# Kernel tuning notes

Measured on AMD Instinct MI355X. Metric: run time of the kernel, lower is better.

Reference implementation:

```python
import jax, jax.numpy as jnp
import numpy as np

N = 500000   # num_nodes
K = 32       # ring buffer slots (max_neighbors)
B = 8192     # event batch size
D = 128      # memory_dim == embedding_dim == attention input_dim
T = 64       # time_dim
H = 2        # num_heads
KS = 16      # top-k sampled neighbors per query


def time_encode(dt, w, b):
    # Time2Vec: sin on even channels, cos on odd channels. dt [...], w/b [T]
    f = dt[..., None] * w + b
    even = (jnp.arange(w.shape[0]) % 2) == 0
    return jnp.where(even, jnp.sin(f), jnp.cos(f))


def setup_inputs() -> dict:
    key = jax.random.key(0)
    ks = jax.random.split(key, 40)
    def rn(i, shape, s=0.05):
        return jax.random.normal(ks[i], shape, dtype=jnp.float32) * s
    inp = {}
    inp["src"] = jax.random.randint(ks[0], (B,), 0, N)
    inp["dst"] = jax.random.randint(ks[1], (B,), 0, N)
    # shift query timestamps so every row has valid (earlier) neighbors w.h.p.
    inp["ts"] = 0.5 + 0.5 * jax.random.uniform(ks[2], (B,), dtype=jnp.float32)
    inp["nbr_ids"] = jax.random.randint(ks[3], (N, K), 0, N, dtype=jnp.int32)
    inp["nbr_ts"] = jax.random.uniform(ks[4], (N, K), dtype=jnp.float32)
    inp["memory"] = rn(5, (N, D), 0.1)
    inp["last_update"] = jnp.zeros((N,), jnp.float32)
    # message function: TimeEncoding + MLP(2*D + T -> D -> D)
    inp["w_t_msg"] = rn(6, (T,), 0.1); inp["b_t_msg"] = jnp.zeros((T,), jnp.float32)
    inp["W_msg1"] = rn(7, (D, 2 * D + T)); inp["b_msg1"] = jnp.zeros((D,), jnp.float32)
    inp["W_msg2"] = rn(8, (D, D)); inp["b_msg2"] = jnp.zeros((D,), jnp.float32)
    # GRUCell(message_dim=D, memory_dim=D)
    inp["W_ih"] = rn(9, (3 * D, D)); inp["b_ih"] = jnp.zeros((3 * D,), jnp.float32)
    inp["W_hh"] = rn(10, (3 * D, D)); inp["b_hh"] = jnp.zeros((3 * D,), jnp.float32)
    # temporal attention
    inp["w_t_att"] = rn(11, (T,), 0.1); inp["b_t_att"] = jnp.zeros((T,), jnp.float32)
    inp["Wq"] = rn(12, (D, D)); inp["bq"] = jnp.zeros((D,), jnp.float32)
    inp["Wk"] = rn(13, (D, D + T)); inp["bk"] = jnp.zeros((D,), jnp.float32)
    inp["Wv"] = rn(14, (D, D + T)); inp["bv"] = jnp.zeros((D,), jnp.float32)
    inp["Wo"] = rn(15, (D, D)); inp["bo"] = jnp.zeros((D,), jnp.float32)
    # merge MLP(D + D -> D -> D) + layernorm
    inp["Wm1"] = rn(16, (D, 2 * D)); inp["bm1"] = jnp.zeros((D,), jnp.float32)
    inp["Wm2"] = rn(17, (D, D)); inp["bm2"] = jnp.zeros((D,), jnp.float32)
    inp["ln_g"] = jnp.ones((D,), jnp.float32); inp["ln_b"] = jnp.zeros((D,), jnp.float32)
    return inp


def reference(src, dst, ts, nbr_ids, nbr_ts, memory, last_update,
              w_t_msg, b_t_msg, W_msg1, b_msg1, W_msg2, b_msg2,
              W_ih, b_ih, W_hh, b_hh,
              w_t_att, b_t_att, Wq, bq, Wk, bk, Wv, bv, Wo, bo,
              Wm1, bm1, Wm2, bm2, ln_g, ln_b):
    # ---- C1: message computation + GRU memory scatter-update (both endpoints) ----
    nodes = jnp.concatenate([src, dst])        # [2B]
    others = jnp.concatenate([dst, src])
    tb = jnp.concatenate([ts, ts])
    self_mem = memory[nodes]                   # [2B, D] gather
    oth_mem = memory[others]
    dt = tb - last_update[nodes]
    te = time_encode(dt, w_t_msg, b_t_msg)     # [2B, T]
    x = jnp.concatenate([self_mem, oth_mem, te], axis=-1)
    msg = jax.nn.relu(x @ W_msg1.T + b_msg1) @ W_msg2.T + b_msg2   # [2B, D]
    # GRUCell
    gi = msg @ W_ih.T + b_ih
    gh = self_mem @ W_hh.T + b_hh
    ir, iz, ig = jnp.split(gi, 3, axis=-1)
    hr, hz, hg = jnp.split(gh, 3, axis=-1)
    r = jax.nn.sigmoid(ir + hr)
    z = jax.nn.sigmoid(iz + hz)
    g = jnp.tanh(ig + r * hg)
    new_mem = (1.0 - z) * g + z * self_mem
    mem2 = memory.at[nodes].set(new_mem)       # scatter-update

    # ---- temporal top-k neighbor sampling for src queries ----
    ids = nbr_ids[src]                         # [B, K]
    nts = nbr_ts[src]                          # [B, K]
    valid = (ids >= 0) & (nts < ts[:, None] + 1e-6)
    sort_ts = jnp.where(valid, nts, -1e30)
    _, idx = jax.lax.top_k(sort_ts, KS)        # most recent first
    sel_ids = jnp.take_along_axis(ids, idx, axis=1)
    sel_ts = jnp.take_along_axis(nts, idx, axis=1)
    mk = jnp.take_along_axis(valid, idx, axis=1)
    tdelta = jnp.where(mk, ts[:, None] - sel_ts, 0.0)
    sel_ids = jnp.clip(jnp.where(mk, sel_ids, 0), 0, N - 1)

    # ---- temporal attention embedding layer ----
    nbr_feat = mem2[sel_ids]                   # [B, KS, D] gather
    node_feat = mem2[src]                      # [B, D]
    te_a = time_encode(tdelta, w_t_att, b_t_att)        # [B, KS, T]
    kv = jnp.concatenate([nbr_feat, te_a], axis=-1)     # [B, KS, D+T]
    hd = D // H
    Q = (node_feat @ Wq.T + bq).reshape(B, H, hd)
    Kp = (kv @ Wk.T + bk).reshape(B, KS, H, hd).transpose(0, 2, 1, 3)
    Vp = (kv @ Wv.T + bv).reshape(B, KS, H, hd).transpose(0, 2, 1, 3)
    scores = jnp.einsum('bhd,bhnd->bhn', Q, Kp) / jnp.sqrt(jnp.float32(hd))
    scores = jnp.where(mk[:, None, :], scores, -jnp.inf)
    attn = jnp.nan_to_num(jax.nn.softmax(scores, axis=-1), nan=0.0)
    out = jnp.einsum('bhn,bhnd->bhd', attn, Vp).reshape(B, D)
    attn_out = out @ Wo.T + bo
    # merge with memory + layernorm
    comb = jnp.concatenate([attn_out, node_feat], axis=-1)
    h = jax.nn.relu(comb @ Wm1.T + bm1) @ Wm2.T + bm2
    mu = h.mean(axis=-1, keepdims=True)
    var = ((h - mu) ** 2).mean(axis=-1, keepdims=True)
    emb = (h - mu) / jnp.sqrt(var + 1e-5) * ln_g + ln_b   # [B, D]
    return emb
```

## Files before the change

### kernel.cpp

```cpp
#include <hip/hip_runtime.h>
#include <math.h>

#define BATCH  8192
#define NNODES 500000
#define DIM    128
#define TDIM   64
#define KNB    32
#define KSEL   16

#define OFF_W1   0
#define OFF_W2   40960
#define OFF_WIH  57344
#define OFF_WHH  106496
#define OFF_WQ   155648
#define OFF_WV   172032
#define OFF_WO   196608
#define OFF_WM1  212992
#define OFF_WM2  245760
#define OFF_WKT  262144
#define CVT_TOT  286720

#define NB_CVT  1120
#define NB_WIN  (NB_CVT + 64)
#define NB_TOPK (NB_WIN + 32)

typedef float  f32x4  __attribute__((ext_vector_type(4)));
typedef __bf16 bf16x8 __attribute__((ext_vector_type(8)));
typedef short  s16x8  __attribute__((ext_vector_type(8)));

#define MFMA(a,b,c) __builtin_amdgcn_mfma_f32_16x16x32_bf16(a,b,c,0,0,0)

__device__ __forceinline__ float rcpf_(float x) { return __builtin_amdgcn_rcpf(x); }
__device__ __forceinline__ float fsigmoid(float x) { return rcpf_(1.f + __expf(-x)); }
__device__ __forceinline__ float ftanh(float x) {
    float e = __expf(2.f * x);
    return 1.f - 2.f * rcpf_(e + 1.f);
}
__device__ __forceinline__ unsigned short f2bf(float x) {
    unsigned u = __builtin_bit_cast(unsigned, x);
    unsigned r = (u + 0x7FFFu + ((u >> 16) & 1u)) >> 16;
    return (unsigned short)r;
}
__device__ __forceinline__ float bf2f(unsigned short u) {
    unsigned v = ((unsigned)u) << 16;
    return __builtin_bit_cast(float, v);
}
__device__ __forceinline__ bf16x8 ldfrag(const unsigned short* p) {
    s16x8 v = *(const s16x8*)p;
    return __builtin_bit_cast(bf16x8, v);
}
__device__ __forceinline__ uint2 pack4bf(float4 v) {
    uint2 pk;
    pk.x = (unsigned)f2bf(v.x) | ((unsigned)f2bf(v.y) << 16);
    pk.y = (unsigned)f2bf(v.z) | ((unsigned)f2bf(v.w) << 16);
    return pk;
}

__global__ __launch_bounds__(256) void k_prep(
    const float* __restrict__ sW1, const float* __restrict__ sW2,
    const float* __restrict__ sWih, const float* __restrict__ sWhh,
    const float* __restrict__ sWq, const float* __restrict__ sWv,
    const float* __restrict__ sWo, const float* __restrict__ sWm1,
    const float* __restrict__ sWm2, const float* __restrict__ sWk,
    unsigned short* __restrict__ pool,
    const int* __restrict__ src, const int* __restrict__ dst,
    int* __restrict__ winner,
    const float* __restrict__ ts,
    const int* __restrict__ nbr_ids, const float* __restrict__ nbr_ts,
    int* __restrict__ sel_id, float* __restrict__ sel_td, int* __restrict__ sel_mk)
{
    const int bid = blockIdx.x;
    const int tid = threadIdx.x;

    if (bid < NB_CVT) {
        int i = bid * 256 + tid;
        float v;
        if      (i < OFF_W2)  { v = sW1 [i - OFF_W1 ]; }
        else if (i < OFF_WIH) { v = sW2 [i - OFF_W2 ]; }
        else if (i < OFF_WHH) { v = sWih[i - OFF_WIH]; }
        else if (i < OFF_WQ)  { v = sWhh[i - OFF_WHH]; }
        else if (i < OFF_WV)  { v = sWq [i - OFF_WQ ]; }
        else if (i < OFF_WO)  { v = sWv [i - OFF_WV ]; }
        else if (i < OFF_WM1) { v = sWo [i - OFF_WO ]; }
        else if (i < OFF_WM2) { v = sWm1[i - OFF_WM1]; }
        else if (i < OFF_WKT) { v = sWm2[i - OFF_WM2]; }
        else {
            int j = i - OFF_WKT;
            int h = j / 12288, rem = j % 12288;
            int c = rem >> 6, dh = rem & 63;
            v = sWk[(size_t)(h * 64 + dh) * 192 + c];
        }
        pool[i] = f2bf(v);
        return;
    }
    if (bid < NB_WIN) {
        int i = (bid - NB_CVT) * 256 + tid;
        if (i < 2 * BATCH) {
            int v = (i < BATCH) ? src[i] : dst[i - BATCH];
            atomicMax(&winner[v], i);
        }
        return;
    }
    {
        int b = (bid - NB_WIN) * 256 + tid;
        if (b >= BATCH) return;
        int   s = src[b];
        float t = ts[b];
        const int4*   ip4 = (const int4*)  (nbr_ids + (size_t)s * KNB);
        const float4* tp4 = (const float4*)(nbr_ts  + (size_t)s * KNB);
        float kt[KNB]; int kid[KNB];
        #pragma unroll
        for (int j4 = 0; j4 < 8; ++j4) {
            int4   id4 = ip4[j4];
            float4 nt4 = tp4[j4];
            int   ids[4] = { id4.x, id4.y, id4.z, id4.w };
            float nts[4] = { nt4.x, nt4.y, nt4.z, nt4.w };
            #pragma unroll
            for (int q = 0; q < 4; ++q) {
                int j = j4 * 4 + q;
                bool valid = (ids[q] >= 0) && (nts[q] < t + 1e-6f);
                kt[j]  = valid ? nts[q] : -1e30f;
                kid[j] = ids[q];
            }
        }
        unsigned picked = 0u;
        for (int sI = 0; sI < KSEL; ++sI) {
            float bv = -3.4e38f; int bj = 0; int bid2 = 0;
            #pragma unroll
            for (int j = 0; j < KNB; ++j) {
                bool avail = !((picked >> j) & 1u);
                if (avail && kt[j] > bv) { bv = kt[j]; bj = j; bid2 = kid[j]; }
            }
            picked |= (1u << bj);
            bool mk = bv > -1e29f;
            int id = mk ? (bid2 < 0 ? 0 : (bid2 > NNODES - 1 ? NNODES - 1 : bid2)) : 0;
            sel_id[b * KSEL + sI] = id;
            sel_td[b * KSEL + sI] = mk ? (t - bv) : 0.f;
            sel_mk[b * KSEL + sI] = mk ? 1 : 0;
        }
    }
}

__global__ __launch_bounds__(512) void k1_mfma(
    const int* __restrict__ src, const int* __restrict__ dst, const float* __restrict__ ts,
    const float* __restrict__ memory, const float* __restrict__ last_update,
    const float* __restrict__ w_t, const float* __restrict__ b_t,
    const unsigned short* __restrict__ Wp,
    const float* __restrict__ b1, const float* __restrict__ b2,
    const float* __restrict__ bih, const float* __restrict__ bhh,
    float* __restrict__ new_mem)
{
    __shared__ unsigned short sxb[64][328];
    __shared__ unsigned short hb [64][136];
    __shared__ int   s_node[64];
    __shared__ int   s_oth [64];
    __shared__ float s_dt  [64];

    const unsigned short* W1b  = Wp + OFF_W1;
    const unsigned short* W2b  = Wp + OFF_W2;
    const unsigned short* Wihb = Wp + OFF_WIH;
    const unsigned short* Whhb = Wp + OFF_WHH;

    const int tid  = threadIdx.x;
    const int base = blockIdx.x * 64;

    if (tid < 64) {
        int gi = base + tid;
        int node, oth; float t;
        if (gi < BATCH) { node = src[gi];         oth = dst[gi];         t = ts[gi]; }
        else            { node = dst[gi - BATCH]; oth = src[gi - BATCH]; t = ts[gi - BATCH]; }
        s_node[tid] = node;
        s_oth[tid]  = oth;
        s_dt[tid]   = t - last_update[node];
    }
    __syncthreads();

    for (int idx = tid; idx < 64 * 32; idx += 512) {
        int r = idx >> 5, c4 = (idx & 31) << 2;
        float4 vs = *(const float4*)&memory[(size_t)s_node[r] * DIM + c4];
        float4 vo = *(const float4*)&memory[(size_t)s_oth[r]  * DIM + c4];
        *(uint2*)&sxb[r][c4]       = pack4bf(vs);
        *(uint2*)&sxb[r][128 + c4] = pack4bf(vo);
    }
    for (int idx = tid; idx < 64 * TDIM; idx += 512) {
        int r = idx >> 6, c = idx & 63;
        float f = s_dt[r] * w_t[c] + b_t[c];
        sxb[r][256 + c] = f2bf((c & 1) ? __cosf(f) : __sinf(f));
    }
    __syncthreads();

    const int w    = tid >> 6;
    const int l    = tid & 63;
    const int rowA = l & 15;
    const int kg   = l >> 4;
    const int n0   = w * 16;
    const int col  = l & 15;
    const int rgrp = l >> 4;

    {
        f32x4 a0 = {0.f,0.f,0.f,0.f}, a1 = {0.f,0.f,0.f,0.f};
        f32x4 a2 = {0.f,0.f,0.f,0.f}, a3 = {0.f,0.f,0.f,0.f};
        #pragma unroll
        for (int kt = 0; kt < 10; ++kt) {
            int ko = kt * 32 + kg * 8;
            bf16x8 bfr = ldfrag(&W1b[(size_t)(n0 + rowA) * 320 + ko]);
            a0 = MFMA(ldfrag(&sxb[     rowA][ko]), bfr, a0);
            a1 = MFMA(ldfrag(&sxb[16 + rowA][ko]), bfr, a1);
            a2 = MFMA(ldfrag(&sxb[32 + rowA][ko]), bfr, a2);
            a3 = MFMA(ldfrag(&sxb[48 + rowA][ko]), bfr, a3);
        }
        float bb = b1[n0 + col];
        #pragma unroll
        for (int rgi = 0; rgi < 4; ++rgi) {
            int rb = rgrp * 4 + rgi;
            hb[rb     ][n0 + col] = f2bf(fmaxf(a0[rgi] + bb, 0.f));
            hb[rb + 16][n0 + col] = f2bf(fmaxf(a1[rgi] + bb, 0.f));
            hb[rb + 32][n0 + col] = f2bf(fmaxf(a2[rgi] + bb, 0.f));
            hb[rb + 48][n0 + col] = f2bf(fmaxf(a3[rgi] + bb, 0.f));
        }
    }
    __syncthreads();

    {
        f32x4 m0 = {0.f,0.f,0.f,0.f}, m1 = {0.f,0.f,0.f,0.f};
        f32x4 m2 = {0.f,0.f,0.f,0.f}, m3 = {0.f,0.f,0.f,0.f};
        #pragma unroll
        for (int kt = 0; kt < 4; ++kt) {
            int ko = kt * 32 + kg * 8;
            bf16x8 bfr = ldfrag(&W2b[(size_t)(n0 + rowA) * 128 + ko]);
            m0 = MFMA(ldfrag(&hb[     rowA][ko]), bfr, m0);
            m1 = MFMA(ldfrag(&hb[16 + rowA][ko]), bfr, m1);
            m2 = MFMA(ldfrag(&hb[32 + rowA][ko]), bfr, m2);
            m3 = MFMA(ldfrag(&hb[48 + rowA][ko]), bfr, m3);
        }
        __syncthreads();
        float bb = b2[n0 + col];
        #pragma unroll
        for (int rgi = 0; rgi < 4; ++rgi) {
            int rb = rgrp * 4 + rgi;
            hb[rb     ][n0 + col] = f2bf(m0[rgi] + bb);
            hb[rb + 16][n0 + col] = f2bf(m1[rgi] + bb);
            hb[rb + 32][n0 + col] = f2bf(m2[rgi] + bb);
            hb[rb + 48][n0 + col] = f2bf(m3[rgi] + bb);
        }
    }
    __syncthreads();

    {
        f32x4 g[6][4];
        #pragma unroll
        for (int gi_ = 0; gi_ < 6; ++gi_)
            #pragma unroll
            for (int ta = 0; ta < 4; ++ta) g[gi_][ta] = (f32x4){0.f,0.f,0.f,0.f};
        #pragma unroll
        for (int kt = 0; kt < 4; ++kt) {
            int ko = kt * 32 + kg * 8;
            int br = n0 + rowA;
            bf16x8 bir = ldfrag(&Wihb[(size_t)(      br) * 128 + ko]);
            bf16x8 biz = ldfrag(&Wihb[(size_t)(128 + br) * 128 + ko]);
            bf16x8 big = ldfrag(&Wihb[(size_t)(256 + br) * 128 + ko]);
            bf16x8 bhr = ldfrag(&Whhb[(size_t)(      br) * 128 + ko]);
            bf16x8 bhz = ldfrag(&Whhb[(size_t)(128 + br) * 128 + ko]);
            bf16x8 bhg = ldfrag(&Whhb[(size_t)(256 + br) * 128 + ko]);
            #pragma unroll
            for (int ta = 0; ta < 4; ++ta) {
                bf16x8 am = ldfrag(&hb [ta * 16 + rowA][ko]);
                bf16x8 ah = ldfrag(&sxb[ta * 16 + rowA][ko]);
                g[0][ta] = MFMA(am, bir, g[0][ta]);
                g[1][ta] = MFMA(am, biz, g[1][ta]);
                g[2][ta] = MFMA(am, big, g[2][ta]);
                g[3][ta] = MFMA(ah, bhr, g[3][ta]);
                g[4][ta] = MFMA(ah, bhz, g[4][ta]);
                g[5][ta] = MFMA(ah, bhg, g[5][ta]);
            }
        }
        const int d = n0 + col;
        float bir = bih[d], biz = bih[128 + d], big = bih[256 + d];
        float bhr = bhh[d], bhz = bhh[128 + d], bhg = bhh[256 + d];
        #pragma unroll
        for (int ta = 0; ta < 4; ++ta)
            #pragma unroll
            for (int rgi = 0; rgi < 4; ++rgi) {
                int rr = ta * 16 + rgrp * 4 + rgi;
                float rv = fsigmoid((g[0][ta][rgi] + bir) + (g[3][ta][rgi] + bhr));
                float zv = fsigmoid((g[1][ta][rgi] + biz) + (g[4][ta][rgi] + bhz));
                float gv = ftanh((g[2][ta][rgi] + big) + rv * (g[5][ta][rgi] + bhg));
                float selfv = bf2f(sxb[rr][d]);
                new_mem[(size_t)(base + rr) * DIM + d] = (1.f - zv) * gv + zv * selfv;
            }
    }
}

__global__ __launch_bounds__(512) void k3_fused(
    const int* __restrict__ src,
    const float* __restrict__ memory, const float* __restrict__ new_mem,
    const int* __restrict__ winner,
    const int* __restrict__ sel_id, const float* __restrict__ sel_td,
    const int* __restrict__ sel_mk,
    const float* __restrict__ w_ta, const float* __restrict__ b_ta,
    const unsigned short* __restrict__ Wp,
    const float* __restrict__ bq, const float* __restrict__ bk,
    const float* __restrict__ bv, const float* __restrict__ bo,
    const float* __restrict__ bm1, const float* __restrict__ bm2,
    const float* __restrict__ ln_g, const float* __restrict__ ln_b,
    float* __restrict__ out)
{
    __shared__ unsigned short s_nfB[32][136];
    __shared__ unsigned short s_qB [32][136];
    __shared__ unsigned short s_u  [32][2][200];
    __shared__ unsigned short s_kvb[32][2][200];
    __shared__ unsigned long long s_pool64[6400];
    __shared__ const float* s_nptr[32][16];
    __shared__ float s_td [32][16];
    __shared__ int   s_mk [32][16];
    __shared__ float s_qb [32][2];
    __shared__ float s_satt[32][2];
    __shared__ float s_at [8][2][16];
    __shared__ const float* s_ptr[32];

    const unsigned short* Wqb  = Wp + OFF_WQ;
    const unsigned short* WkTb = Wp + OFF_WKT;
    const unsigned short* Wvb  = Wp + OFF_WV;
    const unsigned short* Wob  = Wp + OFF_WO;
    const unsigned short* Wm1b = Wp + OFF_WM1;
    const unsigned short* Wm2b = Wp + OFF_WM2;

    const int tid  = threadIdx.x;
    const int base = blockIdx.x * 32;

    if (tid < 32) {
        int v = src[base + tid];
        int wv = winner[v];
        s_ptr[tid] = (wv >= 0) ? (new_mem + (size_t)wv * DIM)
                               : (memory  + (size_t)v  * DIM);
    }
    {
        int r = tid >> 4, n = tid & 15;
        int id = sel_id[(base + r) * KSEL + n];
        int wi = winner[id];
        s_nptr[r][n] = (wi >= 0) ? (new_mem + (size_t)wi * DIM)
                                 : (memory  + (size_t)id * DIM);
        s_td[r][n] = sel_td[(base + r) * KSEL + n];
        s_mk[r][n] = sel_mk[(base + r) * KSEL + n];
    }
    __syncthreads();

    for (int idx = tid; idx < 32 * 32; idx += 512) {
        int r = idx >> 5, c4 = (idx & 31) << 2;
        float4 v = *(const float4*)&s_ptr[r][c4];
        *(uint2*)&s_nfB[r][c4] = pack4bf(v);
    }
    __syncthreads();

    const int w    = tid >> 6;
    const int l    = tid & 63;
    const int rowA = l & 15;
    const int kg   = l >> 4;
    const int col  = l & 15;
    const int rgrp = l >> 4;

    {
        const int n0 = w * 16;
        f32x4 q0 = {0.f,0.f,0.f,0.f}, q1 = {0.f,0.f,0.f,0.f};
        #pragma unroll
        for (int kt = 0; kt < 4; ++kt) {
            int ko = kt * 32 + kg * 8;
            bf16x8 bfr = ldfrag(&Wqb[(size_t)(n0 + rowA) * 128 + ko]);
            q0 = MFMA(ldfrag(&s_nfB[     rowA][ko]), bfr, q0);
            q1 = MFMA(ldfrag(&s_nfB[16 + rowA][ko]), bfr, q1);
        }
        float bb = bq[n0 + col];
        #pragma unroll
        for (int rgi = 0; rgi < 4; ++rgi) {
            int rb = rgrp * 4 + rgi;
            s_qB[rb     ][n0 + col] = f2bf(q0[rgi] + bb);
            s_qB[rb + 16][n0 + col] = f2bf(q1[rgi] + bb);
        }
    }
    __syncthreads();

    if (tid < 256) {
        int r = tid >> 3, rem = tid & 7, h = rem >> 2, p = rem & 3;
        float part = 0.f;
        #pragma unroll
        for (int j = 0; j < 16; ++j) {
            int dd = h * 64 + p * 16 + j;
            part += bf2f(s_qB[r][dd]) * bk[dd];
        }
        part += __shfl_xor(part, 1);
        part += __shfl_xor(part, 2);
        if (p == 0) s_qb[r][h] = part;
    }

    {
        const int h  = w >> 2;
        const int cb = (w & 3) * 48;
        f32x4 u[3][2];
        #pragma unroll
        for (int ct = 0; ct < 3; ++ct)
            #pragma unroll
            for (int ta = 0; ta < 2; ++ta) u[ct][ta] = (f32x4){0.f,0.f,0.f,0.f};
        #pragma unroll
        for (int kt = 0; kt < 2; ++kt) {
            int ko = kt * 32 + kg * 8;
            bf16x8 bfr[3];
            #pragma unroll
            for (int ct = 0; ct < 3; ++ct)
                bfr[ct] = ldfrag(&WkTb[(size_t)h * 12288 + (size_t)(cb + ct * 16 + rowA) * 64 + ko]);
            #pragma unroll
            for (int ta = 0; ta < 2; ++ta) {
                bf16x8 av = ldfrag(&s_qB[ta * 16 + rowA][h * 64 + ko]);
                #pragma unroll
                for (int ct = 0; ct < 3; ++ct)
                    u[ct][ta] = MFMA(av, bfr[ct], u[ct][ta]);
            }
        }
        #pragma unroll
        for (int ct = 0; ct < 3; ++ct)
            #pragma unroll
            for (int ta = 0; ta < 2; ++ta)
                #pragma unroll
                for (int rgi = 0; rgi < 4; ++rgi) {
                    int rr = ta * 16 + rgrp * 4 + rgi;
                    s_u[rr][h][cb + ct * 16 + col] = f2bf(u[ct][ta][rgi]);
                }
    }
    __syncthreads();

    {
        unsigned short (*kvbuf)[16][200] = (unsigned short (*)[16][200])s_pool64;
        float wt = w_ta[l], bt = b_ta[l];
        const int pfn = l >> 5;
        const int pfc = (l & 31) << 2;

        float4 pf[8];
        {
            const int r = w * 4;
            #pragma unroll
            for (int it = 0; it < 8; ++it)
                pf[it] = *(const float4*)&s_nptr[r][it * 2 + pfn][pfc];
        }

        for (int rr = 0; rr < 4; ++rr) {
            const int r = w * 4 + rr;
            #pragma unroll
            for (int it = 0; it < 8; ++it)
                *(uint2*)&kvbuf[w][it * 2 + pfn][pfc] = pack4bf(pf[it]);
            #pragma unroll
            for (int n = 0; n < 16; ++n) {
                float f = s_td[r][n] * wt + bt;
                kvbuf[w][n][128 + l] = f2bf((l & 1) ? __cosf(f) : __sinf(f));
            }
            if (rr < 3) {
                const int rn = r + 1;
                #pragma unroll
                for (int it = 0; it < 8; ++it)
                    pf[it] = *(const float4*)&s_nptr[rn][it * 2 + pfn][pfc];
            }
            __builtin_amdgcn_wave_barrier();

            {
                int h = (l >> 4) & 1, n = l & 15, half = l >> 5;
                float acc = (half == 0) ? s_qb[r][h] : 0.f;
                const unsigned short* kvrow = &kvbuf[w][n][half * 96];
                const unsigned short* urow  = &s_u[r][h][half * 96];
                #pragma unroll
                for (int k = 0; k < 96; k += 8) {
                    s16x8 kv8 = *(const s16x8*)&kvrow[k];
                    s16x8 u8  = *(const s16x8*)&urow[k];
                    #pragma unroll
                    for (int j = 0; j < 8; ++j)
                        acc += bf2f((unsigned short)kv8[j]) * bf2f((unsigned short)u8[j]);
                }
                acc += __shfl_xor(acc, 32);
                int mk = s_mk[r][n];
                float s = mk ? acc * 0.125f : -INFINITY;
                float mx = s;
                #pragma unroll
                for (int m = 1; m < 16; m <<= 1) mx = fmaxf(mx, __shfl_xor(mx, m));
                float p = (mk && mx > -1e37f) ? __expf(s - mx) : 0.f;
                float den = p;
                #pragma unroll
                for (int m = 1; m < 16; m <<= 1) den += __shfl_xor(den, m);
                float a = (den > 0.f) ? (p * rcpf_(den)) : 0.f;
                if (l < 32) s_at[w][h][n] = a;
                if (l == 0 || l == 16) s_satt[r][h] = (den > 0.f) ? 1.f : 0.f;
            }
            __builtin_amdgcn_wave_barrier();

            #pragma unroll
            for (int i = 0; i < 3; ++i) {
                int c = i * 64 + l;
                float k0 = 0.f, k1 = 0.f;
                #pragma unroll
                for (int n = 0; n < 16; ++n) {
                    float v = bf2f(kvbuf[w][n][c]);
                    k0 += s_at[w][0][n] * v;
                    k1 += s_at[w][1][n] * v;
                }
                s_kvb[r][0][c] = f2bf(k0);
                s_kvb[r][1][c] = f2bf(k1);
            }
            __builtin_amdgcn_wave_barrier();
        }
    }
    __syncthreads();

    unsigned short (*s_aoB)[136] = (unsigned short (*)[136])s_pool64;
    unsigned short (*s_oB )[136] = (unsigned short (*)[136])((char*)s_pool64 + 8704);
    unsigned short (*s_h1B)[136] = (unsigned short (*)[136])((char*)s_pool64 + 17408);
    float          (*s_h2 )[128] = (float          (*)[128])((char*)s_pool64 + 26112);

    {
        const int h  = w >> 2;
        const int c0 = (w & 3) * 16;
        f32x4 o0 = {0.f,0.f,0.f,0.f}, o1 = {0.f,0.f,0.f,0.f};
        #pragma unroll
        for (int kt = 0; kt < 6; ++kt) {
            int ko = kt * 32 + kg * 8;
            bf16x8 bfr = ldfrag(&Wvb[(size_t)(h * 64 + c0 + rowA) * 192 + ko]);
            o0 = MFMA(ldfrag(&s_kvb[     rowA][h][ko]), bfr, o0);
            o1 = MFMA(ldfrag(&s_kvb[16 + rowA][h][ko]), bfr, o1);
        }
        int d0 = h * 64 + c0 + col;
        float bv0 = bv[d0];
        #pragma unroll
        for (int rgi = 0; rgi < 4; ++rgi) {
            int rb = rgrp * 4 + rgi;
            s_oB[rb     ][d0] = f2bf(o0[rgi] + s_satt[rb     ][h] * bv0);
            s_oB[rb + 16][d0] = f2bf(o1[rgi] + s_satt[rb + 16][h] * bv0);
        }
    }
    __syncthreads();

    {
        const int n0 = w * 16;
        f32x4 a0 = {0.f,0.f,0.f,0.f}, a1 = {0.f,0.f,0.f,0.f};
        #pragma unroll
        for (int kt = 0; kt < 4; ++kt) {
            int ko = kt * 32 + kg * 8;
            bf16x8 bfr = ldfrag(&Wob[(size_t)(n0 + rowA) * 128 + ko]);
            a0 = MFMA(ldfrag(&s_oB[     rowA][ko]), bfr, a0);
            a1 = MFMA(ldfrag(&s_oB[16 + rowA][ko]), bfr, a1);
        }
        float bb = bo[n0 + col];
        #pragma unroll
        for (int rgi = 0; rgi < 4; ++rgi) {
            int rb = rgrp * 4 + rgi;
            s_aoB[rb     ][n0 + col] = f2bf(a0[rgi] + bb);
            s_aoB[rb + 16][n0 + col] = f2bf(a1[rgi] + bb);
        }
    }
    __syncthreads();

    {
        const int n0 = w * 16;
        f32x4 a0 = {0.f,0.f,0.f,0.f}, a1 = {0.f,0.f,0.f,0.f};
        #pragma unroll
        for (int kt = 0; kt < 8; ++kt) {
            int ko = kt * 32 + kg * 8;
            bf16x8 av0 = (kt < 4) ? ldfrag(&s_aoB[     rowA][ko])
                                  : ldfrag(&s_nfB[     rowA][ko - 128]);
            bf16x8 av1 = (kt < 4) ? ldfrag(&s_aoB[16 + rowA][ko])
                                  : ldfrag(&s_nfB[16 + rowA][ko - 128]);
            bf16x8 bfr = ldfrag(&Wm1b[(size_t)(n0 + rowA) * 256 + ko]);
            a0 = MFMA(av0, bfr, a0);
            a1 = MFMA(av1, bfr, a1);
        }
        float bb = bm1[n0 + col];
        #pragma unroll
        for (int rgi = 0; rgi < 4; ++rgi) {
            int rb = rgrp * 4 + rgi;
            s_h1B[rb     ][n0 + col] = f2bf(fmaxf(a0[rgi] + bb, 0.f));
            s_h1B[rb + 16][n0 + col] = f2bf(fmaxf(a1[rgi] + bb, 0.f));
        }
    }
    __syncthreads();

    {
        const int n0 = w * 16;
        f32x4 a0 = {0.f,0.f,0.f,0.f}, a1 = {0.f,0.f,0.f,0.f};
        #pragma unroll
        for (int kt = 0; kt < 4; ++kt) {
            int ko = kt * 32 + kg * 8;
            bf16x8 bfr = ldfrag(&Wm2b[(size_t)(n0 + rowA) * 128 + ko]);
            a0 = MFMA(ldfrag(&s_h1B[     rowA][ko]), bfr, a0);
            a1 = MFMA(ldfrag(&s_h1B[16 + rowA][ko]), bfr, a1);
        }
        float bb = bm2[n0 + col];
        #pragma unroll
        for (int rgi = 0; rgi < 4; ++rgi) {
            int rb = rgrp * 4 + rgi;
            s_h2[rb     ][n0 + col] = a0[rgi] + bb;
            s_h2[rb + 16][n0 + col] = a1[rgi] + bb;
        }
    }
    __syncthreads();

    {
        float lg0 = ln_g[l], lg1 = ln_g[64 + l];
        float lb0 = ln_b[l], lb1 = ln_b[64 + l];
        #pragma unroll
        for (int i = 0; i < 4; ++i) {
            int r = w * 4 + i;
            float v0 = s_h2[r][l], v1 = s_h2[r][64 + l];
            float sum = v0 + v1;
            #pragma unroll
            for (int m = 1; m < 64; m <<= 1) sum += __shfl_xor(sum, m);
            float mean = sum * (1.f / 128.f);
            float e0 = v0 - mean, e1 = v1 - mean;
            float sq = e0 * e0 + e1 * e1;
            #pragma unroll
            for (int m = 1; m < 64; m <<= 1) sq += __shfl_xor(sq, m);
            float inv = rsqrtf(sq * (1.f / 128.f) + 1e-5f);
            out[(size_t)(base + r) * DIM + l]      = e0 * inv * lg0 + lb0;
            out[(size_t)(base + r) * DIM + 64 + l] = e1 * inv * lg1 + lb1;
        }
    }
}

extern "C" void kernel_launch(void* const* d_in, const int* in_sizes, int n_in,
                              void* d_out, int out_size, void* d_ws, size_t ws_size,
                              hipStream_t stream) {
    const int*   src         = (const int*)  d_in[0];
    const int*   dst         = (const int*)  d_in[1];
    const float* ts          = (const float*)d_in[2];
    const int*   nbr_ids     = (const int*)  d_in[3];
    const float* nbr_ts      = (const float*)d_in[4];
    const float* memory      = (const float*)d_in[5];
    const float* last_update = (const float*)d_in[6];
    const float* w_t_msg     = (const float*)d_in[7];
    const float* b_t_msg     = (const float*)d_in[8];
    const float* W_msg1      = (const float*)d_in[9];
    const float* b_msg1      = (const float*)d_in[10];
    const float* W_msg2      = (const float*)d_in[11];
    const float* b_msg2      = (const float*)d_in[12];
    const float* W_ih        = (const float*)d_in[13];
    const float* b_ih        = (const float*)d_in[14];
    const float* W_hh        = (const float*)d_in[15];
    const float* b_hh        = (const float*)d_in[16];
    const float* w_t_att     = (const float*)d_in[17];
    const float* b_t_att     = (const float*)d_in[18];
    const float* Wq          = (const float*)d_in[19];
    const float* bq          = (const float*)d_in[20];
    const float* Wk          = (const float*)d_in[21];
    const float* bk          = (const float*)d_in[22];
    const float* Wv          = (const float*)d_in[23];
    const float* bv          = (const float*)d_in[24];
    const float* Wo          = (const float*)d_in[25];
    const float* bo          = (const float*)d_in[26];
    const float* Wm1         = (const float*)d_in[27];
    const float* bm1         = (const float*)d_in[28];
    const float* Wm2         = (const float*)d_in[29];
    const float* bm2         = (const float*)d_in[30];
    const float* ln_g        = (const float*)d_in[31];
    const float* ln_b        = (const float*)d_in[32];
    float* out = (float*)d_out;

    char* ws = (char*)d_ws;
    size_t off = 0;
    float* new_mem = (float*)(ws + off); off += (size_t)2 * BATCH * DIM * 4;
    int*   winner  = (int*)  (ws + off); off += 2097152;
    int*   sel_id  = (int*)  (ws + off); off += (size_t)BATCH * KSEL * 4;
    float* sel_td  = (float*)(ws + off); off += (size_t)BATCH * KSEL * 4;
    int*   sel_mk  = (int*)  (ws + off); off += (size_t)BATCH * KSEL * 4;
    unsigned short* Wpool = (unsigned short*)(ws + off); off += (size_t)CVT_TOT * 2;

    hipMemsetAsync(winner, 0xFF, NNODES * sizeof(int), stream);
    k_prep<<<NB_TOPK, 256, 0, stream>>>(
        W_msg1, W_msg2, W_ih, W_hh, Wq, Wv, Wo, Wm1, Wm2, Wk, Wpool,
        src, dst, winner, ts, nbr_ids, nbr_ts, sel_id, sel_td, sel_mk);
    k1_mfma<<<(2 * BATCH) / 64, 512, 0, stream>>>(
        src, dst, ts, memory, last_update,
        w_t_msg, b_t_msg, Wpool, b_msg1, b_msg2, b_ih, b_hh, new_mem);
    k3_fused<<<BATCH / 32, 512, 0, stream>>>(
        src, memory, new_mem, winner, sel_id, sel_td, sel_mk,
        w_t_att, b_t_att, Wpool, bq, bk, bv, bo, bm1, bm2, ln_g, ln_b, out);
}
```

Before: 74.83 us.

## Fold winner init into prep kernel and move scatter/top-k into message kernel

Replaces the separate memset of the winner array with a grid-stride fill inside the weight-conversion kernel. The atomic-max winner scatter and the per-query top-k neighbour selection move from the prep kernel into the first MFMA kernel, done by otherwise idle threads before its main work. This removes one launch and shortens the prep kernel. In exchange the top-k work, which is serial per thread, now runs on the critical path of k1 blocks, and correctness relies on k3 running after k1 in stream order.

New measurement: 72.26 us. 1.04x faster.

```diff
diff --git a/kernel.cpp b/kernel.cpp
--- a/kernel.cpp
+++ b/kernel.cpp
@@ -21,8 +21,6 @@
 #define CVT_TOT  286720
 
 #define NB_CVT  1120
-#define NB_WIN  (NB_CVT + 64)
-#define NB_TOPK (NB_WIN + 32)
 
 typedef float  f32x4  __attribute__((ext_vector_type(4)));
 typedef __bf16 bf16x8 __attribute__((ext_vector_type(8)));
@@ -63,17 +61,10 @@
     const float* __restrict__ sWo, const float* __restrict__ sWm1,
     const float* __restrict__ sWm2, const float* __restrict__ sWk,
     unsigned short* __restrict__ pool,
-    const int* __restrict__ src, const int* __restrict__ dst,
-    int* __restrict__ winner,
-    const float* __restrict__ ts,
-    const int* __restrict__ nbr_ids, const float* __restrict__ nbr_ts,
-    int* __restrict__ sel_id, float* __restrict__ sel_td, int* __restrict__ sel_mk)
+    int* __restrict__ winner)
 {
-    const int bid = blockIdx.x;
-    const int tid = threadIdx.x;
-
-    if (bid < NB_CVT) {
-        int i = bid * 256 + tid;
+    const int i = blockIdx.x * 256 + threadIdx.x;
+    {
         float v;
         if      (i < OFF_W2)  { v = sW1 [i - OFF_W1 ]; }
         else if (i < OFF_WIH) { v = sW2 [i - OFF_W2 ]; }
@@ -91,54 +82,8 @@
             v = sWk[(size_t)(h * 64 + dh) * 192 + c];
         }
         pool[i] = f2bf(v);
-        return;
-    }
-    if (bid < NB_WIN) {
-        int i = (bid - NB_CVT) * 256 + tid;
-        if (i < 2 * BATCH) {
-            int v = (i < BATCH) ? src[i] : dst[i - BATCH];
-            atomicMax(&winner[v], i);
-        }
-        return;
-    }
-    {
-        int b = (bid - NB_WIN) * 256 + tid;
-        if (b >= BATCH) return;
-        int   s = src[b];
-        float t = ts[b];
-        const int4*   ip4 = (const int4*)  (nbr_ids + (size_t)s * KNB);
-        const float4* tp4 = (const float4*)(nbr_ts  + (size_t)s * KNB);
-        float kt[KNB]; int kid[KNB];
-        #pragma unroll
-        for (int j4 = 0; j4 < 8; ++j4) {
-            int4   id4 = ip4[j4];
-            float4 nt4 = tp4[j4];
-            int   ids[4] = { id4.x, id4.y, id4.z, id4.w };
-            float nts[4] = { nt4.x, nt4.y, nt4.z, nt4.w };
-            #pragma unroll
-            for (int q = 0; q < 4; ++q) {
-                int j = j4 * 4 + q;
-                bool valid = (ids[q] >= 0) && (nts[q] < t + 1e-6f);
-                kt[j]  = valid ? nts[q] : -1e30f;
-                kid[j] = ids[q];
-            }
-        }
-        unsigned picked = 0u;
-        for (int sI = 0; sI < KSEL; ++sI) {
-            float bv = -3.4e38f; int bj = 0; int bid2 = 0;
-            #pragma unroll
-            for (int j = 0; j < KNB; ++j) {
-                bool avail = !((picked >> j) & 1u);
-                if (avail && kt[j] > bv) { bv = kt[j]; bj = j; bid2 = kid[j]; }
-            }
-            picked |= (1u << bj);
-            bool mk = bv > -1e29f;
-            int id = mk ? (bid2 < 0 ? 0 : (bid2 > NNODES - 1 ? NNODES - 1 : bid2)) : 0;
-            sel_id[b * KSEL + sI] = id;
-            sel_td[b * KSEL + sI] = mk ? (t - bv) : 0.f;
-            sel_mk[b * KSEL + sI] = mk ? 1 : 0;
-        }
-    }
+    }
+    for (int j = i; j < NNODES; j += NB_CVT * 256) winner[j] = -1;
 }
 
 __global__ __launch_bounds__(512) void k1_mfma(
@@ -148,7 +93,10 @@
     const unsigned short* __restrict__ Wp,
     const float* __restrict__ b1, const float* __restrict__ b2,
     const float* __restrict__ bih, const float* __restrict__ bhh,
-    float* __restrict__ new_mem)
+    float* __restrict__ new_mem,
+    int* __restrict__ winner,
+    const int* __restrict__ nbr_ids, const float* __restrict__ nbr_ts,
+    int* __restrict__ sel_id, float* __restrict__ sel_td, int* __restrict__ sel_mk)
 {
     __shared__ unsigned short sxb[64][328];
     __shared__ unsigned short hb [64][136];
@@ -162,7 +110,50 @@
     const unsigned short* Whhb = Wp + OFF_WHH;
 
     const int tid  = threadIdx.x;
-    const int base = blockIdx.x * 64;
+    const int bid  = blockIdx.x;
+    const int base = bid * 64;
+
+    if (tid < 64) {
+        int i = bid * 64 + tid;
+        int v = (i < BATCH) ? src[i] : dst[i - BATCH];
+        atomicMax(&winner[v], i);
+    } else if (tid < 96) {
+        int b = bid * 32 + (tid - 64);
+        int   s = src[b];
+        float t = ts[b];
+        const int4*   ip4 = (const int4*)  (nbr_ids + (size_t)s * KNB);
+        const float4* tp4 = (const float4*)(nbr_ts  + (size_t)s * KNB);
+        float kt[KNB]; int kid[KNB];
+        #pragma unroll
+        for (int j4 = 0; j4 < 8; ++j4) {
+            int4   id4 = ip4[j4];
+            float4 nt4 = tp4[j4];
+            int   ids[4] = { id4.x, id4.y, id4.z, id4.w };
+            float nts[4] = { nt4.x, nt4.y, nt4.z, nt4.w };
+            #pragma unroll
+            for (int q = 0; q < 4; ++q) {
+                int j = j4 * 4 + q;
+                bool valid = (ids[q] >= 0) && (nts[q] < t + 1e-6f);
+                kt[j]  = valid ? nts[q] : -1e30f;
+                kid[j] = ids[q];
+            }
+        }
+        unsigned picked = 0u;
+        for (int sI = 0; sI < KSEL; ++sI) {
+            float bv = -3.4e38f; int bj = 0; int bid2 = 0;
+            #pragma unroll
+            for (int j = 0; j < KNB; ++j) {
+                bool avail = !((picked >> j) & 1u);
+                if (avail && kt[j] > bv) { bv = kt[j]; bj = j; bid2 = kid[j]; }
+            }
+            picked |= (1u << bj);
+            bool mk = bv > -1e29f;
+            int id = mk ? (bid2 < 0 ? 0 : (bid2 > NNODES - 1 ? NNODES - 1 : bid2)) : 0;
+            sel_id[b * KSEL + sI] = id;
+            sel_td[b * KSEL + sI] = mk ? (t - bv) : 0.f;
+            sel_mk[b * KSEL + sI] = mk ? 1 : 0;
+        }
+    }
 
     if (tid < 64) {
         int gi = base + tid;
@@ -666,13 +657,12 @@
     int*   sel_mk  = (int*)  (ws + off); off += (size_t)BATCH * KSEL * 4;
     unsigned short* Wpool = (unsigned short*)(ws + off); off += (size_t)CVT_TOT * 2;
 
-    hipMemsetAsync(winner, 0xFF, NNODES * sizeof(int), stream);
-    k_prep<<<NB_TOPK, 256, 0, stream>>>(
-        W_msg1, W_msg2, W_ih, W_hh, Wq, Wv, Wo, Wm1, Wm2, Wk, Wpool,
-        src, dst, winner, ts, nbr_ids, nbr_ts, sel_id, sel_td, sel_mk);
+    k_prep<<<NB_CVT, 256, 0, stream>>>(
+        W_msg1, W_msg2, W_ih, W_hh, Wq, Wv, Wo, Wm1, Wm2, Wk, Wpool, winner);
     k1_mfma<<<(2 * BATCH) / 64, 512, 0, stream>>>(
         src, dst, ts, memory, last_update,
-        w_t_msg, b_t_msg, Wpool, b_msg1, b_msg2, b_ih, b_hh, new_mem);
+        w_t_msg, b_t_msg, Wpool, b_msg1, b_msg2, b_ih, b_hh, new_mem,
+        winner, nbr_ids, nbr_ts, sel_id, sel_td, sel_mk);
     k3_fused<<<BATCH / 32, 512, 0, stream>>>(
         src, memory, new_mem, winner, sel_id, sel_td, sel_mk,
         w_t_att, b_t_att, Wpool, bq, bk, bv, bo, bm1, bm2, ln_g, ln_b, out);
```
